# Kernel optimization log

Measured on AMD Instinct MI355X. Metric: run time of the kernel, lower is better.

## Reference

```python
import jax, jax.numpy as jnp
import numpy as np
from jax import lax

RATIOS = np.array([0.5, 1.0, 2.0])
A = 3                      # num anchors per location
K_MIN, K_MAX = 2, 6        # FPN RPN levels
START_SIZE = 32.0          # cfg.FPN.RPN_ANCHOR_START_SIZE
PRE_NMS, POST_NMS = 1000, 1000
NMS_THR = 0.7
FINAL_TOP_N = 1000
BBOX_CLIP = float(np.log(1000.0 / 16.0))


def _whctrs(a):
    w = a[2] - a[0] + 1.0; h = a[3] - a[1] + 1.0
    return w, h, a[0] + 0.5 * (w - 1), a[1] + 0.5 * (h - 1)


def _mkanchors(ws, hs, xc, yc):
    return np.stack([xc - 0.5 * (ws - 1), yc - 0.5 * (hs - 1),
                     xc + 0.5 * (ws - 1), yc + 0.5 * (hs - 1)], axis=1)


def generate_anchors(stride, size):
    # detectron-style: ratio enum on base cell then scale enum
    base = np.array([0.0, 0.0, stride - 1, stride - 1])
    w, h, xc, yc = _whctrs(base)
    szr = (w * h) / RATIOS
    ws = np.round(np.sqrt(szr)); hs = np.round(ws * RATIOS)
    ratio_anchors = _mkanchors(ws, hs, xc, yc)
    scale = size / stride
    out = []
    for i in range(ratio_anchors.shape[0]):
        w, h, xc, yc = _whctrs(ratio_anchors[i])
        out.append(_mkanchors(np.array([w * scale]), np.array([h * scale]), xc, yc))
    return np.vstack(out).astype(np.float32)  # [A,4]


def shifted_anchors(anchors, H, W, stride):
    sx = np.arange(W) * stride; sy = np.arange(H) * stride
    sx, sy = np.meshgrid(sx, sy)
    shifts = np.stack([sx.ravel(), sy.ravel(), sx.ravel(), sy.ravel()], axis=1)
    all_a = shifts[:, None, :] + anchors[None]  # [H*W, A, 4] -> (H,W,A) order
    return jnp.asarray(all_a.reshape(-1, 4).astype(np.float32))


def decode(anchors, deltas):
    w = anchors[:, 2] - anchors[:, 0] + 1.0
    h = anchors[:, 3] - anchors[:, 1] + 1.0
    cx = anchors[:, 0] + 0.5 * w; cy = anchors[:, 1] + 0.5 * h
    dx, dy = deltas[:, 0], deltas[:, 1]
    dw = jnp.minimum(deltas[:, 2], BBOX_CLIP)
    dh = jnp.minimum(deltas[:, 3], BBOX_CLIP)
    pcx = dx * w + cx; pcy = dy * h + cy
    pw = jnp.exp(dw) * w; ph = jnp.exp(dh) * h
    return jnp.stack([pcx - 0.5 * pw, pcy - 0.5 * ph,
                      pcx + 0.5 * pw - 1.0, pcy + 0.5 * ph - 1.0], axis=1)


def clip_boxes(b, imh, imw):
    x1 = jnp.clip(b[:, 0], 0.0, imw - 1.0); y1 = jnp.clip(b[:, 1], 0.0, imh - 1.0)
    x2 = jnp.clip(b[:, 2], 0.0, imw - 1.0); y2 = jnp.clip(b[:, 3], 0.0, imh - 1.0)
    return jnp.stack([x1, y1, x2, y2], axis=1)


def nms_fixed(boxes, scores, thr, max_out):
    # greedy NMS with static trip count; returns keep indices (-1 = invalid)
    N = boxes.shape[0]
    x1, y1, x2, y2 = boxes[:, 0], boxes[:, 1], boxes[:, 2], boxes[:, 3]
    areas = (x2 - x1 + 1.0) * (y2 - y1 + 1.0)
    idx = jnp.arange(N)

    def body(i, st):
        active, keep = st
        s = jnp.where(active, scores, -jnp.inf)
        j = jnp.argmax(s)
        valid = jnp.isfinite(s[j])
        keep = keep.at[i].set(jnp.where(valid, j.astype(jnp.int32), -1))
        xx1 = jnp.maximum(x1[j], x1); yy1 = jnp.maximum(y1[j], y1)
        xx2 = jnp.minimum(x2[j], x2); yy2 = jnp.minimum(y2[j], y2)
        inter = jnp.maximum(0.0, xx2 - xx1 + 1.0) * jnp.maximum(0.0, yy2 - yy1 + 1.0)
        iou = inter / (areas[j] + areas - inter)
        sup = (iou > thr) | (idx == j)
        active = jnp.where(valid, active & ~sup, active)
        return active, keep

    keep0 = jnp.full((max_out,), -1, jnp.int32)
    _, keep = lax.fori_loop(0, max_out, body, (jnp.ones((N,), bool), keep0))
    return keep


def conv(x, w, b, pad):
    y = lax.conv_general_dilated(x, w, (1, 1), [(pad, pad), (pad, pad)],
                                 dimension_numbers=('NCHW', 'OIHW', 'NCHW'))
    return y + b[None, :, None, None]


def level_proposals(probs, deltas, anchors, im_info):
    # probs [B,A,H,W], deltas [B,4A,H,W], anchors [H*W*A,4]
    B, _, H, W = probs.shape

    def per_image(p, d, info):
        s = jnp.transpose(p, (1, 2, 0)).reshape(-1)          # (H,W,A) order
        dl = jnp.transpose(d, (1, 2, 0)).reshape(-1, 4)      # (H,W,A,4)
        k = min(PRE_NMS, s.shape[0])
        ts, ti = lax.top_k(s, k)
        boxes = clip_boxes(decode(anchors[ti], dl[ti]), info[0], info[1])
        keep = nms_fixed(boxes, ts, NMS_THR, min(POST_NMS, k))
        valid = keep >= 0
        kc = jnp.maximum(keep, 0)
        ob = jnp.where(valid[:, None], boxes[kc], 0.0)
        os_ = jnp.where(valid, ts[kc], -1e9)
        pad = POST_NMS - ob.shape[0]
        if pad > 0:
            ob = jnp.pad(ob, ((0, pad), (0, 0)))
            os_ = jnp.pad(os_, (0, pad), constant_values=-1e9)
        return ob, os_

    return jax.vmap(per_image)(probs, deltas, im_info)


def setup_inputs() -> dict:
    key = jax.random.key(0)
    ks = jax.random.split(key, 8)
    d = 256
    shapes = {'feat_p6': (1, d, 16, 16), 'feat_p5': (1, d, 32, 32),
              'feat_p4': (1, d, 64, 64), 'feat_p3': (1, d, 128, 128),
              'feat_p2': (1, d, 256, 256)}
    inp = {n: jax.random.normal(k, sh, jnp.float32)
           for (n, sh), k in zip(shapes.items(), ks[:5])}
    inp['im_info'] = jnp.array([[1024.0, 1024.0, 1.0]], jnp.float32)
    inp['conv_w'] = 0.01 * jax.random.normal(ks[5], (d, d, 3, 3), jnp.float32)
    inp['conv_b'] = jnp.zeros((d,), jnp.float32)
    inp['cls_w'] = 0.01 * jax.random.normal(ks[6], (2 * A, d, 1, 1), jnp.float32)
    inp['cls_b'] = jnp.zeros((2 * A,), jnp.float32)
    inp['bbox_w'] = 0.01 * jax.random.normal(ks[7], (4 * A, d, 1, 1), jnp.float32)
    inp['bbox_b'] = jnp.zeros((4 * A,), jnp.float32)
    return inp


def reference(feat_p6, feat_p5, feat_p4, feat_p3, feat_p2, im_info,
              conv_w, conv_b, cls_w, cls_b, bbox_w, bbox_b):
    feats = [feat_p6, feat_p5, feat_p4, feat_p3, feat_p2]  # blobs_in order (k_max..k_min)
    all_boxes, all_scores = [], []
    for lvl in range(K_MIN, K_MAX + 1):
        x = feats[K_MAX - lvl]
        h = jax.nn.relu(conv(x, conv_w, conv_b, 1))
        cls = conv(h, cls_w, cls_b, 0)      # [B,2A,H,W]
        bbox = conv(h, bbox_w, bbox_b, 0)   # [B,4A,H,W]
        B, C, H, W = cls.shape
        probs = jax.nn.softmax(cls.reshape(B, 2, C // 2, H, W), axis=1)[:, 1]  # [B,A,H,W]
        stride = 2.0 ** lvl
        anc = generate_anchors(stride, START_SIZE * 2.0 ** (lvl - K_MIN))
        anchors = shifted_anchors(anc, H, W, stride)
        b_, s_ = level_proposals(probs, bbox, anchors, im_info)
        all_boxes.append(b_); all_scores.append(s_)
    boxes = jnp.concatenate(all_boxes, axis=1)    # [B, 5*POST_NMS, 4]
    scores = jnp.concatenate(all_scores, axis=1)  # [B, 5*POST_NMS]
    top_s, top_i = lax.top_k(scores, FINAL_TOP_N)
    final_boxes = jnp.take_along_axis(boxes, top_i[:, :, None], axis=1)
    # FPN level assignment (CollectAndDistribute): lvl = 4 + log2(sqrt(area)/224)
    area = ((final_boxes[..., 2] - final_boxes[..., 0] + 1.0) *
            (final_boxes[..., 3] - final_boxes[..., 1] + 1.0))
    scale = jnp.sqrt(jnp.maximum(area, 1.0))
    lvls = jnp.clip(jnp.floor(4.0 + jnp.log2(scale / 224.0 + 1e-6)), 2, 5).astype(jnp.int32)
    return final_boxes, top_s, lvls
```

## Files before the change

### kernel.cpp

```cpp
#include <hip/hip_runtime.h>
#include <math.h>
#include <stdint.h>

typedef unsigned long long u64;
typedef unsigned int u32;

#define CAP 4096
#define NTOT 261888

__device__ __forceinline__ u32 fkey32(float f) {
    u32 u = __float_as_uint(f);
    return (u & 0x80000000u) ? ~u : (u | 0x80000000u);
}

__global__ __launch_bounds__(256) void k_transpose_w(const float* __restrict__ w,
                                                     double* __restrict__ wTd) {
    int t = blockIdx.x * 256 + threadIdx.x;
    if (t >= 2304 * 256) return;
    int kidx = t >> 8;
    int oc = t & 255;
    wTd[t] = (double)w[oc * 2304 + kidx];
}

struct CArgs {
    const float* x[5];
    float* scores[5];
    float* deltas[5];
    const double* wTd;
    const float* cb;
    const float* clsw;
    const float* clsb;
    const float* bbw;
    const float* bbb;
};

__global__ __launch_bounds__(256, 3) void k_conv_heads(CArgs ca) {
    __shared__ __align__(16) float xs[64][3][20];
    __shared__ double hs[256][17];
    __shared__ double hout[18][16];

    int b = blockIdx.x;
    int l, rel;
    if (b < 4096) { l = 0; rel = b; }
    else if (b < 5120) { l = 1; rel = b - 4096; }
    else if (b < 5376) { l = 2; rel = b - 5120; }
    else if (b < 5440) { l = 3; rel = b - 5376; }
    else { l = 4; rel = b - 5440; }
    const int HWs[5] = {256, 128, 64, 32, 16};
    int H = HWs[l], W = H;
    const float* __restrict__ x = ca.x[l];
    float* __restrict__ scores = ca.scores[l];
    float* __restrict__ deltas = ca.deltas[l];
    const double* __restrict__ wTd = ca.wTd;

    int tid = threadIdx.x;
    int pos0 = rel * 16;
    int row = pos0 / W;
    int col0 = pos0 % W;

    double acc[16];
#pragma unroll
    for (int p = 0; p < 16; ++p) acc[p] = 0.0;

    for (int cc = 0; cc < 4; ++cc) {
        __syncthreads();
        for (int t = tid; t < 64 * 3 * 20; t += 256) {
            int a = t / 60;
            int r = t % 60;
            int dy = r / 20;
            int dxx = r % 20;
            float v = 0.f;
            int gy = row - 1 + dy;
            int gx = col0 - 1 + dxx;
            if (dxx < 18 && gy >= 0 && gy < H && gx >= 0 && gx < W)
                v = x[((size_t)(cc * 64 + a) * H + gy) * W + gx];
            xs[a][dy][dxx] = v;
        }
        __syncthreads();
        int oc = tid;
        for (int a = 0; a < 64; ++a) {
#pragma unroll
            for (int dy = 0; dy < 3; ++dy) {
                double xr[18];
#pragma unroll
                for (int q = 0; q < 18; ++q) xr[q] = (double)xs[a][dy][q];
                const double* wrow = &wTd[((size_t)(cc * 64 + a) * 9 + dy * 3) * 256 + oc];
                double w0 = wrow[0];
                double w1 = wrow[256];
                double w2 = wrow[512];
#pragma unroll
                for (int p = 0; p < 16; ++p) {
                    acc[p] = fma(w0, xr[p], acc[p]);
                    acc[p] = fma(w1, xr[p + 1], acc[p]);
                    acc[p] = fma(w2, xr[p + 2], acc[p]);
                }
            }
        }
    }
    __syncthreads();
    {
        double bias = (double)ca.cb[tid];
#pragma unroll
        for (int p = 0; p < 16; ++p) hs[tid][p] = fmax(acc[p] + bias, 0.0);
    }
    __syncthreads();
    for (int t = tid; t < 288; t += 256) {
        int p = t & 15, ch = t >> 4;
        double s = (ch < 6) ? (double)ca.clsb[ch] : (double)ca.bbb[ch - 6];
        const float* __restrict__ wv =
            (ch < 6) ? (ca.clsw + ch * 256) : (ca.bbw + (ch - 6) * 256);
        for (int ci = 0; ci < 256; ++ci) s += (double)wv[ci] * hs[ci][p];
        hout[ch][p] = s;
    }
    __syncthreads();
    for (int t = tid; t < 48; t += 256) {
        int p = t & 15, a = t >> 4;
        int posi = pos0 + p;
        float c0 = (float)hout[a][p], c1 = (float)hout[3 + a][p];
        float m = fmaxf(c0, c1);
        float e0 = expf(__fsub_rn(c0, m));
        float e1 = expf(__fsub_rn(c1, m));
        scores[(size_t)posi * 3 + a] = __fdiv_rn(e1, __fadd_rn(e0, e1));
    }
    for (int t = tid; t < 192; t += 256) {
        int p = t & 15, j = t >> 4;
        int posi = pos0 + p;
        int a = j >> 2, c = j & 3;
        deltas[((size_t)posi * 3 + a) * 4 + c] = (float)hout[6 + j][p];
    }
}

struct SelArgs {
    const float* sc[5];
    u32* h12;
    u32* h24;
    u32* h8;
    u32* selst;
    u32* T32;
    u64* cand;
    u32* ccnt;
    int N[5], K[5];
    int needT[5];
};

__device__ __forceinline__ void lvl_lookup(int g, int& l, int& base) {
    if (g < 196608) { l = 0; base = 0; }
    else if (g < 245760) { l = 1; base = 196608; }
    else if (g < 258048) { l = 2; base = 245760; }
    else if (g < 261120) { l = 3; base = 258048; }
    else { l = 4; base = 261120; }
}

__device__ __forceinline__ void hblk_lookup(int b, int& l, int& base, int& n0) {
    if (b < 48) { l = 0; base = 0; n0 = b * 4096; }
    else if (b < 60) { l = 1; base = 196608; n0 = (b - 48) * 4096; }
    else { l = 2; base = 245760; n0 = (b - 60) * 4096; }
}

__global__ __launch_bounds__(256) void k_zero(SelArgs a) {
    int g = blockIdx.x * 256 + threadIdx.x;
    if (g < 5 * 4096) { a.h12[g] = 0; a.h24[g] = 0; }
    if (g < 5 * 256) a.h8[g] = 0;
    if (g < 5) a.ccnt[g] = 0;
}

__global__ __launch_bounds__(256) void k_h12(SelArgs a) {
    __shared__ u32 hist[4096];
    int l, base, n0;
    hblk_lookup(blockIdx.x, l, base, n0);
    int tid = threadIdx.x;
    for (int i = tid; i < 4096; i += 256) hist[i] = 0;
    __syncthreads();
    const float* sc = a.sc[l];
    int i0 = n0 + tid;
#pragma unroll
    for (int q = 0; q < 16; ++q) {
        u32 key = __float_as_uint(sc[i0 + q * 256]);
        atomicAdd(&hist[key >> 20], 1u);
    }
    __syncthreads();
    for (int i = tid; i < 4096; i += 256) {
        u32 c = hist[i];
        if (c) atomicAdd(&a.h12[l * 4096 + i], c);
    }
}

__global__ __launch_bounds__(1024) void k_sel12(SelArgs a) {
    __shared__ u32 h[4096];
    int l = blockIdx.x;
    if (!a.needT[l]) return;
    for (int i = threadIdx.x; i < 4096; i += 1024) h[i] = a.h12[l * 4096 + i];
    __syncthreads();
    if (threadIdx.x == 0) {
        u32 K = (u32)a.K[l], c = 0;
        for (int b = 4095; b >= 0; --b) {
            c += h[b];
            if (c >= K) {
                a.selst[l * 4 + 0] = (u32)b;
                a.selst[l * 4 + 1] = K - (c - h[b]);
                break;
            }
        }
    }
}

__global__ __launch_bounds__(256) void k_h24(SelArgs a) {
    __shared__ u32 hist[4096];
    int l, base, n0;
    hblk_lookup(blockIdx.x, l, base, n0);
    int tid = threadIdx.x;
    for (int i = tid; i < 4096; i += 256) hist[i] = 0;
    __syncthreads();
    const float* sc = a.sc[l];
    u32 topbin = a.selst[l * 4 + 0];
    int i0 = n0 + tid;
#pragma unroll
    for (int q = 0; q < 16; ++q) {
        u32 key = __float_as_uint(sc[i0 + q * 256]);
        if ((key >> 20) == topbin) atomicAdd(&hist[(key >> 8) & 0xFFFu], 1u);
    }
    __syncthreads();
    for (int i = tid; i < 4096; i += 256) {
        u32 c = hist[i];
        if (c) atomicAdd(&a.h24[l * 4096 + i], c);
    }
}

__global__ __launch_bounds__(1024) void k_sel24(SelArgs a) {
    __shared__ u32 h[4096];
    int l = blockIdx.x;
    if (!a.needT[l]) return;
    for (int i = threadIdx.x; i < 4096; i += 1024) h[i] = a.h24[l * 4096 + i];
    __syncthreads();
    if (threadIdx.x == 0) {
        u32 want = a.selst[l * 4 + 1], c = 0;
        for (int b = 4095; b >= 0; --b) {
            c += h[b];
            if (c >= want) {
                a.selst[l * 4 + 2] = (a.selst[l * 4 + 0] << 12) | (u32)b;
                a.selst[l * 4 + 3] = want - (c - h[b]);
                break;
            }
        }
    }
}

__global__ __launch_bounds__(256) void k_h8(SelArgs a) {
    int g = blockIdx.x * 256 + threadIdx.x;
    if (g >= NTOT) return;
    int l, base;
    lvl_lookup(g, l, base);
    if (!a.needT[l]) return;
    u32 key = __float_as_uint(a.sc[l][g - base]);
    if ((key >> 8) == a.selst[l * 4 + 2])
        atomicAdd(&a.h8[l * 256 + (key & 0xFFu)], 1u);
}

__global__ __launch_bounds__(256) void k_sel8(SelArgs a) {
    __shared__ u32 h[256];
    int l = blockIdx.x;
    if (!a.needT[l]) {
        if (threadIdx.x == 0) a.T32[l] = 0u;
        return;
    }
    if (threadIdx.x < 256) h[threadIdx.x] = a.h8[l * 256 + threadIdx.x];
    __syncthreads();
    if (threadIdx.x == 0) {
        u32 want = a.selst[l * 4 + 3], c = 0;
        for (int b = 255; b >= 0; --b) {
            c += h[b];
            if (c >= want) {
                a.T32[l] = (a.selst[l * 4 + 2] << 8) | (u32)b;
                break;
            }
        }
    }
}

__global__ __launch_bounds__(256) void k_compact(SelArgs a) {
    int g = blockIdx.x * 256 + threadIdx.x;
    if (g >= NTOT) return;
    int l, base;
    lvl_lookup(g, l, base);
    int i = g - base;
    u32 key = __float_as_uint(a.sc[l][i]);
    bool pred = (key >= a.T32[l]);
    u64 mask = __ballot(pred);
    int lane = threadIdx.x & 63;
    u32 cnt = (u32)__popcll(mask);
    u32 basep = 0;
    if (cnt) {
        int leader = __ffsll((long long)mask) - 1;
        if (lane == leader) basep = atomicAdd(&a.ccnt[l], cnt);
        basep = __shfl(basep, leader);
    }
    if (pred) {
        u32 off = (u32)__popcll(mask & ((1ull << lane) - 1ull));
        u32 p = basep + off;
        if (p < CAP) a.cand[l * CAP + p] = ((u64)key << 32) | (u32)(~(u32)i);
    }
}

struct TArgs {
    const u64* cand;
    const u32* ccnt;
    const float* dl[5];
    float* ts[5];
    float* boxes[5];
    float* areas[5];
    int K[5], W[5];
    float stride[5];
    float anc[5][12];
    const float* im_info;
};

__global__ __launch_bounds__(1024) void k_sortdecode(TArgs a) {
    __shared__ u64 sk[CAP];
    int l = blockIdx.x;
    int tid = threadIdx.x;
    u32 cnt = a.ccnt[l];
    if (cnt > CAP) cnt = CAP;
    for (int i = tid; i < CAP; i += 1024)
        sk[i] = (i < (int)cnt) ? a.cand[l * CAP + i] : 0ull;
    __syncthreads();
    for (int k2 = 2; k2 <= CAP; k2 <<= 1)
        for (int j = k2 >> 1; j > 0; j >>= 1) {
            for (int i = tid; i < CAP; i += 1024) {
                int p2 = i ^ j;
                if (p2 > i) {
                    u64 va = sk[i], vb = sk[p2];
                    if ((va < vb) == ((i & k2) == 0)) {
                        sk[i] = vb;
                        sk[p2] = va;
                    }
                }
            }
            __syncthreads();
        }
    int K = a.K[l];
    float imh = a.im_info[0], imw = a.im_info[1];
    float hi_x = __fsub_rn(imw, 1.0f), hi_y = __fsub_rn(imh, 1.0f);
    if (tid < K) {
        u64 v = sk[tid];
        u32 idx = ~(u32)(v & 0xffffffffu);
        float score = __uint_as_float((u32)(v >> 32));
        a.ts[l][tid] = score;
        int aidx = idx % 3;
        int posi = idx / 3;
        int W = a.W[l];
        int rr = posi / W, cc = posi % W;
        float sx = __fmul_rn((float)cc, a.stride[l]);
        float sy = __fmul_rn((float)rr, a.stride[l]);
        const float* an = &a.anc[l][aidx * 4];
        float ax1 = __fadd_rn(an[0], sx), ay1 = __fadd_rn(an[1], sy);
        float ax2 = __fadd_rn(an[2], sx), ay2 = __fadd_rn(an[3], sy);
        float w = __fadd_rn(__fsub_rn(ax2, ax1), 1.0f);
        float h = __fadd_rn(__fsub_rn(ay2, ay1), 1.0f);
        float cx = __fadd_rn(ax1, __fmul_rn(0.5f, w));
        float cy = __fadd_rn(ay1, __fmul_rn(0.5f, h));
        const float* d = &a.dl[l][(size_t)idx * 4];
        float dx = d[0], dy = d[1];
        float dw = fminf(d[2], 4.135166556742356f);
        float dh = fminf(d[3], 4.135166556742356f);
        float pcx = __fadd_rn(__fmul_rn(dx, w), cx);
        float pcy = __fadd_rn(__fmul_rn(dy, h), cy);
        float pw = __fmul_rn(expf(dw), w);
        float ph = __fmul_rn(expf(dh), h);
        float hw2 = __fmul_rn(0.5f, pw), hh2 = __fmul_rn(0.5f, ph);
        float x1 = __fsub_rn(pcx, hw2);
        float y1 = __fsub_rn(pcy, hh2);
        float x2 = __fsub_rn(__fadd_rn(pcx, hw2), 1.0f);
        float y2 = __fsub_rn(__fadd_rn(pcy, hh2), 1.0f);
        x1 = fminf(fmaxf(x1, 0.0f), hi_x);
        y1 = fminf(fmaxf(y1, 0.0f), hi_y);
        x2 = fminf(fmaxf(x2, 0.0f), hi_x);
        y2 = fminf(fmaxf(y2, 0.0f), hi_y);
        float* obx = &a.boxes[l][(size_t)tid * 4];
        obx[0] = x1;
        obx[1] = y1;
        obx[2] = x2;
        obx[3] = y2;
        a.areas[l][tid] = __fmul_rn(__fadd_rn(__fsub_rn(x2, x1), 1.0f),
                                    __fadd_rn(__fsub_rn(y2, y1), 1.0f));
    }
}

struct IArgs {
    const float* boxes[5];
    const float* areas[5];
    u64* sup[5];
    int K[5];
};

__global__ __launch_bounds__(256) void k_iou(IArgs a) {
    int bx = blockIdx.x;
    int l = bx / 1000;
    int i = bx % 1000;
    int K = a.K[l];
    if (i >= K) return;
    const float* bi = &a.boxes[l][(size_t)i * 4];
    float x1 = bi[0], y1 = bi[1], x2 = bi[2], y2 = bi[3];
    float ai = a.areas[l][i];
    int lane = threadIdx.x & 63;
    int wv = threadIdx.x >> 6;
#pragma unroll
    for (int it = 0; it < 4; ++it) {
        int j = it * 256 + wv * 64 + lane;
        bool sup = false;
        if (j > i && j < K) {
            const float* bj = &a.boxes[l][(size_t)j * 4];
            float xx1 = fmaxf(x1, bj[0]);
            float yy1 = fmaxf(y1, bj[1]);
            float xx2 = fminf(x2, bj[2]);
            float yy2 = fminf(y2, bj[3]);
            float iw = fmaxf(0.0f, __fadd_rn(__fsub_rn(xx2, xx1), 1.0f));
            float ih = fmaxf(0.0f, __fadd_rn(__fsub_rn(yy2, yy1), 1.0f));
            float inter = __fmul_rn(iw, ih);
            float uni = __fsub_rn(__fadd_rn(ai, a.areas[l][j]), inter);
            float iou = __fdiv_rn(inter, uni);
            sup = iou > 0.7f;
        }
        u64 m = __ballot(sup);
        if (lane == 0) a.sup[l][(size_t)i * 16 + it * 4 + wv] = m;
    }
}

struct GArgs {
    const u64* sup[5];
    int K[5];
    int* keep[5];
    int* nkeep[5];
};

__global__ __launch_bounds__(64) void k_nms_scan(GArgs a) {
    int l = blockIdx.x;
    int K = a.K[l];
    const u64* __restrict__ sup = a.sup[l];
    int lane = threadIdx.x;
    bool owner = lane < 16;
    u64 mask = 0ull;
    int nk = 0;
    int* keep = a.keep[l];
    u64 r[16];
#pragma unroll
    for (int q = 0; q < 16; ++q)
        r[q] = (owner && q < K) ? sup[(size_t)q * 16 + lane] : 0ull;
    for (int i0 = 0; i0 < K; i0 += 16) {
#pragma unroll
        for (int q = 0; q < 16; ++q) {
            int i = i0 + q;
            if (i < K) {
                u64 w = __shfl(mask, i >> 6);
                bool suppressed = (w >> (i & 63)) & 1ull;
                u64 rowv = r[q];
                int nxt = i + 16;
                r[q] = (owner && nxt < K) ? sup[(size_t)nxt * 16 + lane] : 0ull;
                if (!suppressed) {
                    if (lane == 0) keep[nk] = i;
                    ++nk;
                    mask |= rowv;
                }
            }
        }
    }
    if (lane == 0) *a.nkeep[l] = nk;
}

struct EArgs {
    const float* ts[5];
    const float* boxes[5];
    const int* keep[5];
    const int* nkeep[5];
    float* ob;
    float* os;
};

__global__ __launch_bounds__(256) void k_emit(EArgs a) {
    int l = blockIdx.x;
    int nk = *a.nkeep[l];
    for (int r = threadIdx.x; r < 1000; r += 256) {
        float b0 = 0, b1 = 0, b2 = 0, b3 = 0, s = -1000000000.0f;
        if (r < nk) {
            int j = a.keep[l][r];
            const float* bp = &a.boxes[l][(size_t)j * 4];
            b0 = bp[0];
            b1 = bp[1];
            b2 = bp[2];
            b3 = bp[3];
            s = a.ts[l][j];
        }
        float* op = &a.ob[(size_t)(l * 1000 + r) * 4];
        op[0] = b0;
        op[1] = b1;
        op[2] = b2;
        op[3] = b3;
        a.os[l * 1000 + r] = s;
    }
}

__global__ __launch_bounds__(1024) void k_final(const float* __restrict__ ob,
                                                const float* __restrict__ os,
                                                float* __restrict__ out) {
    __shared__ u64 sk[8192];
    int tid = threadIdx.x;
    for (int i = tid; i < 8192; i += 1024)
        sk[i] = (i < 5000) ? (((u64)fkey32(os[i]) << 32) | (u32)(~(u32)i)) : 0ull;
    __syncthreads();
    for (int k2 = 2; k2 <= 8192; k2 <<= 1)
        for (int j = k2 >> 1; j > 0; j >>= 1) {
            for (int i = tid; i < 8192; i += 1024) {
                int p2 = i ^ j;
                if (p2 > i) {
                    u64 va = sk[i], vb = sk[p2];
                    if ((va < vb) == ((i & k2) == 0)) {
                        sk[i] = vb;
                        sk[p2] = va;
                    }
                }
            }
            __syncthreads();
        }
    if (tid < 1000) {
        u64 v = sk[tid];
        u32 gi = ~(u32)(v & 0xffffffffu);
        float s = os[gi];
        const float* b = &ob[(size_t)gi * 4];
        float x1 = b[0], y1 = b[1], x2 = b[2], y2 = b[3];
        out[tid * 4 + 0] = x1;
        out[tid * 4 + 1] = y1;
        out[tid * 4 + 2] = x2;
        out[tid * 4 + 3] = y2;
        out[4000 + tid] = s;
        float area = __fmul_rn(__fadd_rn(__fsub_rn(x2, x1), 1.0f),
                               __fadd_rn(__fsub_rn(y2, y1), 1.0f));
        float scale = __fsqrt_rn(fmaxf(area, 1.0f));
        float t = __fadd_rn(__fdiv_rn(scale, 224.0f), 1e-6f);
        float lv = floorf(__fadd_rn(4.0f, log2f(t)));
        lv = fminf(fmaxf(lv, 2.0f), 5.0f);
        out[5000 + tid] = lv;
    }
}

extern "C" void kernel_launch(void* const* d_in, const int* in_sizes, int n_in,
                              void* d_out, int out_size, void* d_ws, size_t ws_size,
                              hipStream_t stream) {
    const float *fp2 = nullptr, *fp3 = nullptr, *fp4 = nullptr, *fp5 = nullptr, *fp6 = nullptr;
    const float *im_info = nullptr, *conv_w = nullptr, *conv_b = nullptr;
    const float *cls_w = nullptr, *cls_b = nullptr, *bbox_w = nullptr, *bbox_b = nullptr;
    for (int i = 0; i < n_in; ++i) {
        const float* p = (const float*)d_in[i];
        switch (in_sizes[i]) {
            case 16777216: fp2 = p; break;
            case 4194304: fp3 = p; break;
            case 1048576: fp4 = p; break;
            case 262144: fp5 = p; break;
            case 65536: fp6 = p; break;
            case 3: im_info = p; break;
            case 589824: conv_w = p; break;
            case 256: conv_b = p; break;
            case 1536: cls_w = p; break;
            case 6: cls_b = p; break;
            case 3072: bbox_w = p; break;
            case 12: bbox_b = p; break;
            default: break;
        }
    }
    const float* feats[5] = {fp2, fp3, fp4, fp5, fp6};

    size_t off = 0;
    auto take = [&](size_t bytes) -> void* {
        void* p = (char*)d_ws + off;
        off += (bytes + 255) & ~(size_t)255;
        return p;
    };
    double* wTd = (double*)take((size_t)2304 * 256 * 8);
    int Hs[5] = {256, 128, 64, 32, 16};
    float* scores[5];
    float* deltas[5];
    float* ts[5];
    float* boxes[5];
    float* areas[5];
    int* keep[5];
    int* nkeep[5];
    u64* sup[5];
    int Narr[5], Karr[5];
    for (int s = 0; s < 5; ++s) {
        int H = Hs[s];
        int N = 3 * H * H;
        Narr[s] = N;
        Karr[s] = N < 1000 ? N : 1000;
        scores[s] = (float*)take((size_t)N * 4);
        deltas[s] = (float*)take((size_t)N * 16);
        ts[s] = (float*)take(1024 * 4);
        boxes[s] = (float*)take(1024 * 16);
        areas[s] = (float*)take(1024 * 4);
        keep[s] = (int*)take(1024 * 4);
        nkeep[s] = (int*)take(256);
        sup[s] = (u64*)take((size_t)1000 * 16 * 8);
    }
    float* ob = (float*)take((size_t)5000 * 16);
    float* os = (float*)take((size_t)5000 * 4);
    u32* h12 = (u32*)take(5 * 4096 * 4);
    u32* h24 = (u32*)take(5 * 4096 * 4);
    u32* h8 = (u32*)take(5 * 256 * 4);
    u32* selst = (u32*)take(5 * 4 * 4);
    u32* T32 = (u32*)take(5 * 4);
    u64* cand = (u64*)take((size_t)5 * CAP * 8);
    u32* ccnt = (u32*)take(5 * 4);

    double anc[5][12];
    for (int s = 0; s < 5; ++s) {
        int lvl = 2 + s;
        double stride = (double)(1 << lvl);
        double xc = 0.5 * (stride - 1.0);
        const double ratios[3] = {0.5, 1.0, 2.0};
        for (int rr = 0; rr < 3; ++rr) {
            double wsv = rint(sqrt(stride * stride / ratios[rr]));
            double hsv = rint(wsv * ratios[rr]);
            double WS = wsv * 8.0, HS = hsv * 8.0;
            anc[s][rr * 4 + 0] = xc - 0.5 * (WS - 1.0);
            anc[s][rr * 4 + 1] = xc - 0.5 * (HS - 1.0);
            anc[s][rr * 4 + 2] = xc + 0.5 * (WS - 1.0);
            anc[s][rr * 4 + 3] = xc + 0.5 * (HS - 1.0);
        }
    }

    k_transpose_w<<<dim3(2304), dim3(256), 0, stream>>>(conv_w, wTd);

    CArgs ca;
    for (int s = 0; s < 5; ++s) {
        ca.x[s] = feats[s];
        ca.scores[s] = scores[s];
        ca.deltas[s] = deltas[s];
    }
    ca.wTd = wTd;
    ca.cb = conv_b;
    ca.clsw = cls_w;
    ca.clsb = cls_b;
    ca.bbw = bbox_w;
    ca.bbb = bbox_b;
    k_conv_heads<<<dim3(5456), dim3(256), 0, stream>>>(ca);

    SelArgs sa;
    TArgs a2;
    IArgs a3;
    GArgs a4;
    EArgs a5;
    for (int s = 0; s < 5; ++s) {
        sa.sc[s] = scores[s];
        sa.N[s] = Narr[s];
        sa.K[s] = Karr[s];
        sa.needT[s] = (Narr[s] > CAP) ? 1 : 0;
        a2.dl[s] = deltas[s];
        a2.ts[s] = ts[s];
        a2.boxes[s] = boxes[s];
        a2.areas[s] = areas[s];
        a2.K[s] = Karr[s];
        a2.W[s] = Hs[s];
        a2.stride[s] = (float)(1 << (2 + s));
        for (int q = 0; q < 12; ++q) a2.anc[s][q] = (float)anc[s][q];
        a3.boxes[s] = boxes[s];
        a3.areas[s] = areas[s];
        a3.sup[s] = sup[s];
        a3.K[s] = Karr[s];
        a4.sup[s] = sup[s];
        a4.K[s] = Karr[s];
        a4.keep[s] = keep[s];
        a4.nkeep[s] = nkeep[s];
        a5.ts[s] = ts[s];
        a5.boxes[s] = boxes[s];
        a5.keep[s] = keep[s];
        a5.nkeep[s] = nkeep[s];
    }
    sa.h12 = h12;
    sa.h24 = h24;
    sa.h8 = h8;
    sa.selst = selst;
    sa.T32 = T32;
    sa.cand = cand;
    sa.ccnt = ccnt;
    a2.cand = cand;
    a2.ccnt = ccnt;
    a2.im_info = im_info;
    a5.ob = ob;
    a5.os = os;

    int fb = (NTOT + 255) / 256;
    k_zero<<<dim3((5 * 4096 + 255) / 256), dim3(256), 0, stream>>>(sa);
    k_h12<<<dim3(63), dim3(256), 0, stream>>>(sa);
    k_sel12<<<dim3(5), dim3(1024), 0, stream>>>(sa);
    k_h24<<<dim3(63), dim3(256), 0, stream>>>(sa);
    k_sel24<<<dim3(5), dim3(1024), 0, stream>>>(sa);
    k_h8<<<dim3(fb), dim3(256), 0, stream>>>(sa);
    k_sel8<<<dim3(5), dim3(256), 0, stream>>>(sa);
    k_compact<<<dim3(fb), dim3(256), 0, stream>>>(sa);
    k_sortdecode<<<dim3(5), dim3(1024), 0, stream>>>(a2);
    k_iou<<<dim3(5000), dim3(256), 0, stream>>>(a3);
    k_nms_scan<<<dim3(5), dim3(64), 0, stream>>>(a4);
    k_emit<<<dim3(5), dim3(256), 0, stream>>>(a5);
    k_final<<<dim3(1), dim3(1024), 0, stream>>>(ob, os, (float*)d_out);
}
```

Before: 3.255 ms.

## Pack conv weights as double4, store input tile as double, shrink head shared memory

The 3x3 conv weights are repacked so each (channel, row) triple of taps sits in one padded 4-double slot per output channel, letting one vector load plus one scalar load fetch all three taps. The input tile is converted to double once when staged into shared memory and read back as double2, which removes per-use float-to-double conversions. The 1x1 head is now computed in four passes of four positions each, shrinking the hidden-activation buffer so the occupancy hint can rise from 3 to 4 blocks. The trade-off is extra synchronisation in the head stage, a larger input tile in shared memory and a weight buffer with padding.

```diff
diff --git a/kernel.cpp b/kernel.cpp
--- a/kernel.cpp
+++ b/kernel.cpp
@@ -14,19 +14,24 @@
 }
 
 __global__ __launch_bounds__(256) void k_transpose_w(const float* __restrict__ w,
-                                                     double* __restrict__ wTd) {
+                                                     double* __restrict__ wT4) {
     int t = blockIdx.x * 256 + threadIdx.x;
-    if (t >= 2304 * 256) return;
-    int kidx = t >> 8;
+    if (t >= 768 * 256) return;
+    int r = t >> 8;
     int oc = t & 255;
-    wTd[t] = (double)w[oc * 2304 + kidx];
+    double* dst = &wT4[(size_t)t * 4];
+    const float* src = &w[(size_t)oc * 2304 + r * 3];
+    dst[0] = (double)src[0];
+    dst[1] = (double)src[1];
+    dst[2] = (double)src[2];
+    dst[3] = 0.0;
 }
 
 struct CArgs {
     const float* x[5];
     float* scores[5];
     float* deltas[5];
-    const double* wTd;
+    const double* wT4;
     const float* cb;
     const float* clsw;
     const float* clsb;
@@ -34,10 +39,10 @@
     const float* bbb;
 };
 
-__global__ __launch_bounds__(256, 3) void k_conv_heads(CArgs ca) {
-    __shared__ __align__(16) float xs[64][3][20];
-    __shared__ double hs[256][17];
-    __shared__ double hout[18][16];
+__global__ __launch_bounds__(256, 4) void k_conv_heads(CArgs ca) {
+    __shared__ __align__(16) double xs[64][3][20];
+    __shared__ double hsh[256][4];
+    __shared__ float hout[18][16];
 
     int b = blockIdx.x;
     int l, rel;
@@ -51,7 +56,7 @@
     const float* __restrict__ x = ca.x[l];
     float* __restrict__ scores = ca.scores[l];
     float* __restrict__ deltas = ca.deltas[l];
-    const double* __restrict__ wTd = ca.wTd;
+    const double* __restrict__ wT4 = ca.wT4;
 
     int tid = threadIdx.x;
     int pos0 = rel * 16;
@@ -74,7 +79,7 @@
             int gx = col0 - 1 + dxx;
             if (dxx < 18 && gy >= 0 && gy < H && gx >= 0 && gx < W)
                 v = x[((size_t)(cc * 64 + a) * H + gy) * W + gx];
-            xs[a][dy][dxx] = v;
+            xs[a][dy][dxx] = (double)v;
         }
         __syncthreads();
         int oc = tid;
@@ -82,12 +87,19 @@
 #pragma unroll
             for (int dy = 0; dy < 3; ++dy) {
                 double xr[18];
-#pragma unroll
-                for (int q = 0; q < 18; ++q) xr[q] = (double)xs[a][dy][q];
-                const double* wrow = &wTd[((size_t)(cc * 64 + a) * 9 + dy * 3) * 256 + oc];
-                double w0 = wrow[0];
-                double w1 = wrow[256];
-                double w2 = wrow[512];
+                const double2* xp = (const double2*)&xs[a][dy][0];
+#pragma unroll
+                for (int q = 0; q < 9; ++q) {
+                    double2 v2 = xp[q];
+                    xr[2 * q] = v2.x;
+                    xr[2 * q + 1] = v2.y;
+                }
+                int ridx = (cc * 64 + a) * 3 + dy;
+                const double* wrow = &wT4[((size_t)ridx * 256 + oc) * 4];
+                double2 w01 = *(const double2*)wrow;
+                double w0 = w01.x;
+                double w1 = w01.y;
+                double w2 = wrow[2];
 #pragma unroll
                 for (int p = 0; p < 16; ++p) {
                     acc[p] = fma(w0, xr[p], acc[p]);
@@ -97,26 +109,26 @@
             }
         }
     }
-    __syncthreads();
-    {
-        double bias = (double)ca.cb[tid];
-#pragma unroll
-        for (int p = 0; p < 16; ++p) hs[tid][p] = fmax(acc[p] + bias, 0.0);
-    }
-    __syncthreads();
-    for (int t = tid; t < 288; t += 256) {
-        int p = t & 15, ch = t >> 4;
-        double s = (ch < 6) ? (double)ca.clsb[ch] : (double)ca.bbb[ch - 6];
-        const float* __restrict__ wv =
-            (ch < 6) ? (ca.clsw + ch * 256) : (ca.bbw + (ch - 6) * 256);
-        for (int ci = 0; ci < 256; ++ci) s += (double)wv[ci] * hs[ci][p];
-        hout[ch][p] = s;
+    double bias = (double)ca.cb[tid];
+    for (int qh = 0; qh < 4; ++qh) {
+        __syncthreads();
+#pragma unroll
+        for (int p = 0; p < 4; ++p) hsh[tid][p] = fmax(acc[qh * 4 + p] + bias, 0.0);
+        __syncthreads();
+        for (int t = tid; t < 72; t += 256) {
+            int p = t & 3, ch = t >> 2;
+            double s = (ch < 6) ? (double)ca.clsb[ch] : (double)ca.bbb[ch - 6];
+            const float* __restrict__ wv =
+                (ch < 6) ? (ca.clsw + ch * 256) : (ca.bbw + (ch - 6) * 256);
+            for (int ci = 0; ci < 256; ++ci) s += (double)wv[ci] * hsh[ci][p];
+            hout[ch][qh * 4 + p] = (float)s;
+        }
     }
     __syncthreads();
     for (int t = tid; t < 48; t += 256) {
         int p = t & 15, a = t >> 4;
         int posi = pos0 + p;
-        float c0 = (float)hout[a][p], c1 = (float)hout[3 + a][p];
+        float c0 = hout[a][p], c1 = hout[3 + a][p];
         float m = fmaxf(c0, c1);
         float e0 = expf(__fsub_rn(c0, m));
         float e1 = expf(__fsub_rn(c1, m));
@@ -126,7 +138,7 @@
         int p = t & 15, j = t >> 4;
         int posi = pos0 + p;
         int a = j >> 2, c = j & 3;
-        deltas[((size_t)posi * 3 + a) * 4 + c] = (float)hout[6 + j][p];
+        deltas[((size_t)posi * 3 + a) * 4 + c] = hout[6 + j][p];
     }
 }
 
@@ -573,7 +585,7 @@
         off += (bytes + 255) & ~(size_t)255;
         return p;
     };
-    double* wTd = (double*)take((size_t)2304 * 256 * 8);
+    double* wT4 = (double*)take((size_t)768 * 256 * 4 * 8);
     int Hs[5] = {256, 128, 64, 32, 16};
     float* scores[5];
     float* deltas[5];
@@ -624,22 +636,6 @@
             anc[s][rr * 4 + 3] = xc + 0.5 * (HS - 1.0);
         }
     }
-
-    k_transpose_w<<<dim3(2304), dim3(256), 0, stream>>>(conv_w, wTd);
-
-    CArgs ca;
-    for (int s = 0; s < 5; ++s) {
-        ca.x[s] = feats[s];
-        ca.scores[s] = scores[s];
-        ca.deltas[s] = deltas[s];
-    }
-    ca.wTd = wTd;
-    ca.cb = conv_b;
-    ca.clsw = cls_w;
-    ca.clsb = cls_b;
-    ca.bbw = bbox_w;
-    ca.bbb = bbox_b;
-    k_conv_heads<<<dim3(5456), dim3(256), 0, stream>>>(ca);
 
     SelArgs sa;
     TArgs a2;
@@ -685,8 +681,24 @@
     a5.ob = ob;
     a5.os = os;
 
+    k_transpose_w<<<dim3(768), dim3(256), 0, stream>>>(conv_w, wT4);
+    k_zero<<<dim3((5 * 4096 + 255) / 256), dim3(256), 0, stream>>>(sa);
+
+    CArgs ca;
+    for (int s = 0; s < 5; ++s) {
+        ca.x[s] = feats[s];
+        ca.scores[s] = scores[s];
+        ca.deltas[s] = deltas[s];
+    }
+    ca.wT4 = wT4;
+    ca.cb = conv_b;
+    ca.clsw = cls_w;
+    ca.clsb = cls_b;
+    ca.bbw = bbox_w;
+    ca.bbb = bbox_b;
+    k_conv_heads<<<dim3(5456), dim3(256), 0, stream>>>(ca);
+
     int fb = (NTOT + 255) / 256;
-    k_zero<<<dim3((5 * 4096 + 255) / 256), dim3(256), 0, stream>>>(sa);
     k_h12<<<dim3(63), dim3(256), 0, stream>>>(sa);
     k_sel12<<<dim3(5), dim3(1024), 0, stream>>>(sa);
     k_h24<<<dim3(63), dim3(256), 0, stream>>>(sa);
```

Result: no change. 3.197 ms (-1.8%).
